# Optimization experiments

Hardware: AMD Instinct MI355X
Metric: run time of the kernel (lower is better)

The kernel has to match this reference:

```python
import jax, jax.numpy as jnp
import numpy as np

PLANES, RATIO = 512, 4
Q = PLANES // RATIO  # 128
B, H, W = 4, 128, 128


def _dw_stride2(x, k):
    # depthwise 3x3 stride-2 conv, NCHW, kernel [C,1,3,3]
    return jax.lax.conv_general_dilated(
        x, k, window_strides=(2, 2), padding=((1, 1), (1, 1)),
        feature_group_count=x.shape[1],
        dimension_numbers=('NCHW', 'OIHW', 'NCHW'))


def _upsample_bilinear_ac(x, out_h, out_w):
    # bilinear, align_corners=True (matches F.interpolate)
    n, c, h, w = x.shape
    def co(out, ins):
        s = (ins - 1) / (out - 1)
        pos = jnp.arange(out, dtype=jnp.float32) * jnp.float32(s)
        i0 = jnp.floor(pos).astype(jnp.int32)
        i1 = jnp.minimum(i0 + 1, ins - 1)
        return i0, i1, pos - i0.astype(jnp.float32)
    y0, y1, ty = co(out_h, h)
    x0, x1, tx = co(out_w, w)
    rows = x[:, :, y0, :] * (1 - ty)[None, None, :, None] + x[:, :, y1, :] * ty[None, None, :, None]
    return rows[:, :, :, x0] * (1 - tx) + rows[:, :, :, x1] * tx


def setup_inputs() -> dict:
    key = jax.random.key(0)
    ks = jax.random.split(key, 32)
    nrm = lambda k, s, sc=0.05: jax.random.normal(k, s, jnp.float32) * sc
    uni = lambda k, s: jax.random.uniform(k, s, jnp.float32, 0.5, 1.5)
    return {
        'feat': jax.random.normal(ks[0], (B, PLANES, H, W), jnp.float32),
        'w_phi': nrm(ks[1], (2 * Q, PLANES)),
        'bn_phi_s': uni(ks[2], (2 * Q,)), 'bn_phi_b': nrm(ks[3], (2 * Q,)),
        'w_theta': nrm(ks[4], (Q, PLANES)),
        'bn_theta_s': uni(ks[5], (Q,)), 'bn_theta_b': nrm(ks[6], (Q,)),
        'w_adj': nrm(ks[7], (Q, Q)),
        'bn_adj_s': uni(ks[8], (Q,)), 'bn_adj_b': nrm(ks[9], (Q,)),
        'w_wg': nrm(ks[10], (2 * Q, 2 * Q)),
        'bn_wg_s': uni(ks[11], (2 * Q,)), 'bn_wg_b': nrm(ks[12], (2 * Q,)),
        'w_conv3': nrm(ks[13], (PLANES, 2 * Q)),
        'bn3_s': uni(ks[14], (PLANES,)), 'bn3_b': nrm(ks[15], (PLANES,)),
        'w_local1': nrm(ks[16], (PLANES, 1, 3, 3), 0.2),
        'bnl1_s': uni(ks[17], (PLANES,)), 'bnl1_b': nrm(ks[18], (PLANES,)),
        'w_local2': nrm(ks[19], (PLANES, 1, 3, 3), 0.2),
        'bnl2_s': uni(ks[20], (PLANES,)), 'bnl2_b': nrm(ks[21], (PLANES,)),
        'w_local3': nrm(ks[22], (PLANES, 1, 3, 3), 0.2),
        'bnl3_s': uni(ks[23], (PLANES,)), 'bnl3_b': nrm(ks[24], (PLANES,)),
        'gamma': nrm(ks[25], (1,), 0.5),
        'w_final': nrm(ks[26], (PLANES, 2 * PLANES)),
        'bnf_s': uni(ks[27], (PLANES,)), 'bnf_b': nrm(ks[28], (PLANES,)),
    }


def reference(feat, w_phi, bn_phi_s, bn_phi_b, w_theta, bn_theta_s, bn_theta_b,
              w_adj, bn_adj_s, bn_adj_b, w_wg, bn_wg_s, bn_wg_b,
              w_conv3, bn3_s, bn3_b,
              w_local1, bnl1_s, bnl1_b, w_local2, bnl2_s, bnl2_b,
              w_local3, bnl3_s, bnl3_b, gamma, w_final, bnf_s, bnf_b):
    n, c, h, w = feat.shape
    bn2 = lambda x, s, b: x * s[None, :, None, None] + b[None, :, None, None]
    bn1 = lambda x, s, b: x * s[None, :, None] + b[None, :, None]
    conv1x1 = lambda x, wt: jnp.einsum('oc,nchw->nohw', wt, x)

    l = bn2(_dw_stride2(feat, w_local1), bnl1_s, bnl1_b)
    l = bn2(_dw_stride2(l, w_local2), bnl2_s, bnl2_b)
    l = bn2(_dw_stride2(l, w_local3), bnl3_s, bnl3_b)
    nl, cl, hl, wl = l.shape
    v = l.reshape(nl, cl, hl * wl)                      # [n,C,hw]
    energy = jnp.einsum('nck,ndk->ncd', v, v)           # [n,C,C]
    attn = jax.nn.softmax(jnp.max(energy, -1, keepdims=True) - energy, axis=-1)
    cam = jnp.einsum('ncd,ndk->nck', attn, v).reshape(nl, cl, hl, wl)
    l = gamma * cam + l
    local = _upsample_bilinear_ac(l, h, w)
    spatial_local_feat = feat * local + feat

    # ---- graph branch
    q = w_theta.shape[0]
    x_sqz = bn2(conv1x1(feat, w_phi), bn_phi_s, bn_phi_b).reshape(n, 2 * q, h * w)
    b_m = bn2(conv1x1(feat, w_theta), bn_theta_s, bn_theta_b).reshape(n, q, h * w)
    z_idt = jnp.einsum('nck,ndk->ncd', x_sqz, b_m)      # [n,2q,q]
    z = jnp.swapaxes(z_idt, 1, 2)                       # [n,q,2q]
    z = bn1(jnp.einsum('oi,nil->nol', w_adj, z), bn_adj_s, bn_adj_b)
    z = jnp.swapaxes(z, 1, 2) + z_idt                   # [n,2q,q]
    z = bn1(jnp.einsum('oi,nil->nol', w_wg, z), bn_wg_s, bn_wg_b)
    y = jnp.einsum('ncd,ndk->nck', z, b_m).reshape(n, 2 * q, h, w)
    y = bn2(conv1x1(y, w_conv3), bn3_s, bn3_b)
    g_out = jax.nn.relu(feat + y)

    out = bn2(conv1x1(jnp.concatenate([spatial_local_feat, g_out], axis=1), w_final), bnf_s, bnf_b)
    return out
```

## Files before the change

### kernel.cpp

```cpp
#include <hip/hip_runtime.h>
#include <hip/hip_bf16.h>
#include <cstddef>
#include <cstdint>

static constexpr int NB  = 4;
static constexpr int CH  = 512;
static constexpr int HH  = 128;
static constexpr int WWi = 128;
static constexpr int HW  = HH * WWi;
static constexpr int Qd  = 128;
static constexpr int Q2d = 256;

typedef __attribute__((ext_vector_type(8))) short bf8;
typedef __attribute__((ext_vector_type(4))) float f4;

__device__ __forceinline__ short f2bf(float x) {
  __hip_bfloat16 h = __float2bfloat16(x);
  short s; __builtin_memcpy(&s, &h, 2); return s;
}
__device__ __forceinline__ float bfs2f(short u) {
  union { unsigned int i; float f; } x;
  x.i = ((unsigned int)(unsigned short)u) << 16; return x.f;
}

__launch_bounds__(256)
__global__ void dw_conv_bn(const float* __restrict__ in, float* __restrict__ out,
                           const float* __restrict__ wgt, const float* __restrict__ s,
                           const float* __restrict__ b, int Hi, int Wi, int Ho, int Wo) {
  int idx = blockIdx.x * 256 + threadIdx.x;
  int wo = idx % Wo; int t = idx / Wo;
  int ho = t % Ho; t /= Ho;
  int c = t % CH; int n = t / CH;
  const float* ip = in + ((size_t)(n * CH + c)) * Hi * Wi;
  const float* wp = wgt + c * 9;
  float acc = 0.f;
  int hi = ho * 2 - 1, wi = wo * 2 - 1;
#pragma unroll
  for (int kh = 0; kh < 3; kh++) {
    int y = hi + kh;
    if ((unsigned)y < (unsigned)Hi) {
#pragma unroll
      for (int kw = 0; kw < 3; kw++) {
        int x = wi + kw;
        if ((unsigned)x < (unsigned)Wi) acc += wp[kh * 3 + kw] * ip[y * Wi + x];
      }
    }
  }
  out[idx] = acc * s[c] + b[c];
}

__launch_bounds__(256)
__global__ void lrow_kernel(const float* __restrict__ lcam, float* __restrict__ lrow) {
  int idx = blockIdx.x * 256 + threadIdx.x;
  int wcol = idx & 127; int t = idx >> 7;
  int hy = t & 15; t >>= 4;
  float pos = wcol * (15.f / 127.f);
  int x0 = (int)pos; if (x0 > 15) x0 = 15;
  float tx = pos - x0;
  int x1 = x0 + 1; if (x1 > 15) x1 = 15;
  const float* lc = lcam + ((size_t)t * 16 + hy) * 16;
  lrow[idx] = lc[x0] * (1.f - tx) + lc[x1] * tx;
}

__launch_bounds__(256)
__global__ void cvt_f32_bf16(const float* __restrict__ in, short* __restrict__ out, int n4) {
  int i = blockIdx.x * 256 + threadIdx.x;
  if (i >= n4) return;
  float4 v = ((const float4*)in)[i];
  short tmp[4] = {f2bf(v.x), f2bf(v.y), f2bf(v.z), f2bf(v.w)};
  short4 o; __builtin_memcpy(&o, tmp, 8);
  ((short4*)out)[i] = o;
}

__device__ __forceinline__ int sls(int row, int slot) {
  return row * 64 + ((slot ^ (((row >> 1) ^ (row >> 3)) & 7)) << 3);
}
__device__ __forceinline__ void stg64_b16(const short* __restrict__ src, size_t stride,
                                          int kb, short* lds, int t) {
#pragma unroll
  for (int i = 0; i < 4; i++) {
    int chunk = t + i * 256;
    int row = chunk >> 3, slot = chunk & 7;
    bf8 v = *(const bf8*)(src + (size_t)row * stride + kb + slot * 8);
    *(bf8*)(lds + sls(row, slot)) = v;
  }
}
__device__ __forceinline__ void stg64_f32(const float* __restrict__ src, size_t stride,
                                          int kb, short* lds, int t) {
#pragma unroll
  for (int i = 0; i < 4; i++) {
    int chunk = t + i * 256;
    int row = chunk >> 3, slot = chunk & 7;
    const float* sp = src + (size_t)row * stride + kb + slot * 8;
    float4 v0 = *(const float4*)sp, v1 = *(const float4*)(sp + 4);
    union { short s[8]; bf8 v; } u;
    u.s[0] = f2bf(v0.x); u.s[1] = f2bf(v0.y); u.s[2] = f2bf(v0.z); u.s[3] = f2bf(v0.w);
    u.s[4] = f2bf(v1.x); u.s[5] = f2bf(v1.y); u.s[6] = f2bf(v1.z); u.s[7] = f2bf(v1.w);
    *(bf8*)(lds + sls(row, slot)) = u.v;
  }
}
__device__ __forceinline__ void stg64_t32(const float* __restrict__ src, size_t sstride,
                                          int pb, short* lds, int t) {
#pragma unroll
  for (int i2 = 0; i2 < 4; i2++) {
    int chunk = t + i2 * 256;
    int c = (chunk >> 3) & 63;
    int p8 = ((chunk & 7) | ((chunk >> 6) & 8)) * 8;
    const float* fr = src + (size_t)c * sstride + pb + p8;
    float4 f0 = *(const float4*)fr, f1 = *(const float4*)(fr + 4);
    float fv[8];
    __builtin_memcpy(&fv[0], &f0, 16); __builtin_memcpy(&fv[4], &f1, 16);
    int slot = c >> 3, eidx = c & 7;
#pragma unroll
    for (int e = 0; e < 8; e++) {
      lds[sls(p8 + e, slot) + eidx] = f2bf(fv[e]);
    }
  }
}
__device__ __forceinline__ void stg64_t16(const short* __restrict__ src, size_t sstride,
                                          int pb, short* lds, int t) {
#pragma unroll
  for (int i2 = 0; i2 < 4; i2++) {
    int chunk = t + i2 * 256;
    int c = (chunk >> 3) & 63;
    int p8 = ((chunk & 7) | ((chunk >> 6) & 8)) * 8;
    bf8 v = *(const bf8*)(src + (size_t)c * sstride + pb + p8);
    int slot = c >> 3, eidx = c & 7;
#pragma unroll
    for (int e = 0; e < 8; e++) {
      lds[sls(p8 + e, slot) + eidx] = v[e];
    }
  }
}
__device__ __forceinline__ bf8 fragld64(const short* lds, int row, int kk, int lg) {
  return *(const bf8*)(lds + sls(row, kk * 4 + lg));
}

__launch_bounds__(256)
__global__ void energy_mfma(const float* __restrict__ l3, float* __restrict__ energy) {
  const int c0 = blockIdx.x * 128;
  const int d0 = blockIdx.y * 128;
  const int n = blockIdx.z;
  const int t = threadIdx.x;
  const int lane16 = t & 15, lg = (t >> 4) & 3, wave = t >> 6;
  const int wm = (wave >> 1) * 64, wn = (wave & 1) * 64;
  __shared__ __align__(16) short lA[8192], lB[8192];
  const float* srcA = l3 + ((size_t)n * CH + c0) * 256;
  const float* srcB = l3 + ((size_t)n * CH + d0) * 256;
  f4 acc[4][4];
#pragma unroll
  for (int i = 0; i < 4; i++)
#pragma unroll
    for (int j = 0; j < 4; j++) acc[i][j] = (f4)0.f;
  for (int kb = 0; kb < 256; kb += 64) {
    stg64_f32(srcA, 256, kb, lA, t);
    stg64_f32(srcB, 256, kb, lB, t);
    __syncthreads();
#pragma unroll
    for (int kk = 0; kk < 2; kk++) {
      bf8 av[4], bv[4];
#pragma unroll
      for (int i = 0; i < 4; i++) av[i] = fragld64(lA, wm + i * 16 + lane16, kk, lg);
#pragma unroll
      for (int j = 0; j < 4; j++) bv[j] = fragld64(lB, wn + j * 16 + lane16, kk, lg);
#pragma unroll
      for (int i = 0; i < 4; i++)
#pragma unroll
        for (int j = 0; j < 4; j++)
          acc[i][j] = __builtin_amdgcn_mfma_f32_16x16x32_bf16(av[i], bv[j], acc[i][j], 0, 0, 0);
    }
    __syncthreads();
  }
#pragma unroll
  for (int i = 0; i < 4; i++)
#pragma unroll
    for (int j = 0; j < 4; j++) {
      int d = d0 + wn + j * 16 + lane16;
#pragma unroll
      for (int r = 0; r < 4; r++) {
        int c = c0 + wm + i * 16 + lg * 4 + r;
        energy[((size_t)n * CH + c) * CH + d] = acc[i][j][r];
      }
    }
}

__launch_bounds__(256)
__global__ void softmax_attn(float* __restrict__ energy) {
  float* row = energy + (size_t)blockIdx.x * CH;
  int t = threadIdx.x;
  __shared__ float red[256];
  float e0 = row[t], e1 = row[t + 256];
  red[t] = fminf(e0, e1);
  __syncthreads();
  for (int s = 128; s > 0; s >>= 1) {
    if (t < s) red[t] = fminf(red[t], red[t + s]);
    __syncthreads();
  }
  float emin = red[0];
  __syncthreads();
  float w0 = __expf(emin - e0), w1 = __expf(emin - e1);
  red[t] = w0 + w1;
  __syncthreads();
  for (int s = 128; s > 0; s >>= 1) {
    if (t < s) red[t] += red[t + s];
    __syncthreads();
  }
  float inv = 1.f / red[0];
  row[t] = w0 * inv;
  row[t + 256] = w1 * inv;
}

__launch_bounds__(256)
__global__ void cam_mfma(const float* __restrict__ attn, const float* __restrict__ l3,
                         const float* __restrict__ gamma, float* __restrict__ lcam) {
  const int pb = blockIdx.x * 128;
  const int mb = blockIdx.y * 128;
  const int n = blockIdx.z;
  const int t = threadIdx.x;
  const int lane16 = t & 15, lg = (t >> 4) & 3, wave = t >> 6;
  const int wm = (wave >> 1) * 64, wn = (wave & 1) * 64;
  __shared__ __align__(16) short lA[8192], lB[8192];
  const float* srcA = attn + ((size_t)n * CH + mb) * CH;
  const float gm = gamma[0];
  f4 acc[4][4];
#pragma unroll
  for (int i = 0; i < 4; i++)
#pragma unroll
    for (int j = 0; j < 4; j++) acc[i][j] = (f4)0.f;
  for (int kb = 0; kb < 512; kb += 64) {
    stg64_f32(srcA, CH, kb, lA, t);
    stg64_t32(l3 + ((size_t)n * CH + kb) * 256, 256, pb, lB, t);
    __syncthreads();
#pragma unroll
    for (int kk = 0; kk < 2; kk++) {
      bf8 av[4], bv[4];
#pragma unroll
      for (int i = 0; i < 4; i++) av[i] = fragld64(lA, wm + i * 16 + lane16, kk, lg);
#pragma unroll
      for (int j = 0; j < 4; j++) bv[j] = fragld64(lB, wn + j * 16 + lane16, kk, lg);
#pragma unroll
      for (int i = 0; i < 4; i++)
#pragma unroll
        for (int j = 0; j < 4; j++)
          acc[i][j] = __builtin_amdgcn_mfma_f32_16x16x32_bf16(av[i], bv[j], acc[i][j], 0, 0, 0);
    }
    __syncthreads();
  }
#pragma unroll
  for (int i = 0; i < 4; i++)
#pragma unroll
    for (int j = 0; j < 4; j++) {
      int p = pb + wn + j * 16 + lane16;
#pragma unroll
      for (int r = 0; r < 4; r++) {
        int c = mb + wm + i * 16 + lg * 4 + r;
        size_t idx = ((size_t)n * CH + c) * 256 + p;
        lcam[idx] = gm * acc[i][j][r] + l3[idx];
      }
    }
}

__launch_bounds__(256)
__global__ void theta_mfma2(const short* __restrict__ wthb, const float* __restrict__ feat,
                            const float* __restrict__ s, const float* __restrict__ b,
                            short* __restrict__ bmb) {
  const int pb = blockIdx.x * 128;
  const int n = blockIdx.y;
  const int t = threadIdx.x;
  const int lane16 = t & 15, lg = (t >> 4) & 3, wave = t >> 6;
  const int wm = (wave >> 1) * 64, wn = (wave & 1) * 64;
  __shared__ __align__(16) short lA[8192], lB[8192];
  f4 acc[4][4];
#pragma unroll
  for (int i = 0; i < 4; i++)
#pragma unroll
    for (int j = 0; j < 4; j++) acc[i][j] = (f4)0.f;
  for (int kb = 0; kb < 512; kb += 64) {
    stg64_b16(wthb, 512, kb, lA, t);
    stg64_t32(feat + ((size_t)(n * CH) + kb) * HW, HW, pb, lB, t);
    __syncthreads();
#pragma unroll
    for (int kk = 0; kk < 2; kk++) {
      bf8 av[4], bv[4];
#pragma unroll
      for (int i = 0; i < 4; i++) av[i] = fragld64(lA, wm + i * 16 + lane16, kk, lg);
#pragma unroll
      for (int j = 0; j < 4; j++) bv[j] = fragld64(lB, wn + j * 16 + lane16, kk, lg);
#pragma unroll
      for (int i = 0; i < 4; i++)
#pragma unroll
        for (int j = 0; j < 4; j++)
          acc[i][j] = __builtin_amdgcn_mfma_f32_16x16x32_bf16(av[i], bv[j], acc[i][j], 0, 0, 0);
    }
    __syncthreads();
  }
#pragma unroll
  for (int i = 0; i < 4; i++)
#pragma unroll
    for (int j = 0; j < 4; j++) {
      int p = pb + wn + j * 16 + lane16;
#pragma unroll
      for (int r = 0; r < 4; r++) {
        int d = wm + i * 16 + lg * 4 + r;
        bmb[((size_t)(n * Qd) + d) * HW + p] = f2bf(s[d] * acc[i][j][r] + b[d]);
      }
    }
}

__launch_bounds__(256)
__global__ void rowsum_bf(const short* __restrict__ bmb, float* __restrict__ rs) {
  int row = blockIdx.x;
  int t = threadIdx.x;
  const short* r = bmb + (size_t)row * HW;
  float a = 0.f;
  for (int p = t * 8; p < HW; p += 2048) {
    bf8 v = *(const bf8*)(r + p);
#pragma unroll
    for (int e = 0; e < 8; e++) a += bfs2f(v[e]);
  }
  __shared__ float red[256];
  red[t] = a;
  __syncthreads();
  for (int s = 128; s > 0; s >>= 1) {
    if (t < s) red[t] += red[t + s];
    __syncthreads();
  }
  if (t == 0) rs[row] = red[0];
}

__launch_bounds__(256)
__global__ void m1_mfma2(const float* __restrict__ feat, const short* __restrict__ bmb,
                         float* __restrict__ m1p) {
  const int c0 = blockIdx.x * 128;
  const int kc = blockIdx.y;
  const int n = blockIdx.z;
  const int t = threadIdx.x;
  const int lane16 = t & 15, lg = (t >> 4) & 3, wave = t >> 6;
  const int wm = (wave >> 1) * 64, wn = (wave & 1) * 64;
  __shared__ __align__(16) short lA[8192], lB[8192];
  const float* srcA = feat + ((size_t)(n * CH) + c0) * HW;
  const short* srcB = bmb + (size_t)(n * Qd) * HW;
  f4 acc[4][4];
#pragma unroll
  for (int i = 0; i < 4; i++)
#pragma unroll
    for (int j = 0; j < 4; j++) acc[i][j] = (f4)0.f;
  const int kend = kc * 1024 + 1024;
  for (int kb = kc * 1024; kb < kend; kb += 64) {
    stg64_f32(srcA, HW, kb, lA, t);
    stg64_b16(srcB, HW, kb, lB, t);
    __syncthreads();
#pragma unroll
    for (int kk = 0; kk < 2; kk++) {
      bf8 av[4], bv[4];
#pragma unroll
      for (int i = 0; i < 4; i++) av[i] = fragld64(lA, wm + i * 16 + lane16, kk, lg);
#pragma unroll
      for (int j = 0; j < 4; j++) bv[j] = fragld64(lB, wn + j * 16 + lane16, kk, lg);
#pragma unroll
      for (int i = 0; i < 4; i++)
#pragma unroll
        for (int j = 0; j < 4; j++)
          acc[i][j] = __builtin_amdgcn_mfma_f32_16x16x32_bf16(av[i], bv[j], acc[i][j], 0, 0, 0);
    }
    __syncthreads();
  }
#pragma unroll
  for (int i = 0; i < 4; i++)
#pragma unroll
    for (int j = 0; j < 4; j++) {
      int d = wn + j * 16 + lane16;
#pragma unroll
      for (int r = 0; r < 4; r++) {
        int c = c0 + wm + i * 16 + lg * 4 + r;
        m1p[(((size_t)kc * NB + n) * CH + c) * Qd + d] = acc[i][j][r];
      }
    }
}

__launch_bounds__(256)
__global__ void m1_reduce(const float* __restrict__ m1p, float* __restrict__ m1) {
  int idx = blockIdx.x * 256 + threadIdx.x;
  float a = 0.f;
#pragma unroll
  for (int kc = 0; kc < 16; kc++) a += m1p[(size_t)kc * (NB * CH * Qd) + idx];
  m1[idx] = a;
}

__launch_bounds__(128)
__global__ void zidt_kernel(const float* __restrict__ m1, const float* __restrict__ wphi,
                            const float* __restrict__ sp, const float* __restrict__ bp,
                            const float* __restrict__ rs, float* __restrict__ zidt) {
  int n = blockIdx.y, c = blockIdx.x, d = threadIdx.x;
  __shared__ float wrow[512];
  for (int i = d; i < 512; i += 128) wrow[i] = wphi[(size_t)c * 512 + i];
  __syncthreads();
  const float* mb = m1 + (size_t)n * CH * Qd;
  float acc = 0.f;
#pragma unroll 4
  for (int i = 0; i < 512; i++) acc += wrow[i] * mb[i * Qd + d];
  zidt[((size_t)n * Q2d + c) * Qd + d] = sp[c] * acc + bp[c] * rs[n * Qd + d];
}

__launch_bounds__(128)
__global__ void z3_kernel(const float* __restrict__ zidt, const float* __restrict__ wadj,
                          const float* __restrict__ sa, const float* __restrict__ ba,
                          float* __restrict__ z3) {
  int n = blockIdx.y, c = blockIdx.x, d = threadIdx.x;
  __shared__ float zr[128];
  zr[d] = zidt[((size_t)n * Q2d + c) * Qd + d];
  __syncthreads();
  const float* wrow = wadj + (size_t)d * 128;
  float acc = 0.f;
#pragma unroll 4
  for (int i = 0; i < 128; i++) acc += wrow[i] * zr[i];
  z3[((size_t)n * Q2d + c) * Qd + d] = sa[d] * acc + ba[d] + zr[d];
}

__launch_bounds__(128)
__global__ void z4_kernel(const float* __restrict__ z3, const float* __restrict__ wwg,
                          const float* __restrict__ sw, const float* __restrict__ bw,
                          float* __restrict__ z4) {
  int n = blockIdx.y, o = blockIdx.x, d = threadIdx.x;
  __shared__ float wrow[256];
  wrow[d] = wwg[(size_t)o * 256 + d];
  wrow[d + 128] = wwg[(size_t)o * 256 + 128 + d];
  __syncthreads();
  const float* zb = z3 + (size_t)n * Q2d * Qd;
  float acc = 0.f;
#pragma unroll 4
  for (int i = 0; i < 256; i++) acc += wrow[i] * zb[i * Qd + d];
  z4[((size_t)n * Q2d + o) * Qd + d] = sw[o] * acc + bw[o];
}

__launch_bounds__(128)
__global__ void wz_kernel(const float* __restrict__ z4, const float* __restrict__ wc3,
                          const float* __restrict__ s3, float* __restrict__ wz) {
  int n = blockIdx.y, o = blockIdx.x, d = threadIdx.x;
  __shared__ float wrow[256];
  wrow[d] = wc3[(size_t)o * 256 + d];
  wrow[d + 128] = wc3[(size_t)o * 256 + 128 + d];
  __syncthreads();
  const float* zb = z4 + (size_t)n * Q2d * Qd;
  float acc = 0.f;
#pragma unroll 4
  for (int i = 0; i < 256; i++) acc += wrow[i] * zb[i * Qd + d];
  wz[((size_t)n * CH + o) * Qd + d] = s3[o] * acc;
}

__launch_bounds__(256)
__global__ void ygout_mfma2(const float* __restrict__ wz, const short* __restrict__ bmb,
                            const float* __restrict__ feat, const float* __restrict__ b3,
                            short* __restrict__ gout) {
  const int pb = blockIdx.x * 128;
  const int mb = blockIdx.y * 128;
  const int n = blockIdx.z;
  const int t = threadIdx.x;
  const int lane16 = t & 15, lg = (t >> 4) & 3, wave = t >> 6;
  const int wm = (wave >> 1) * 64, wn = (wave & 1) * 64;
  __shared__ __align__(16) short lA[8192], lB[8192];
  const float* srcA = wz + ((size_t)(n * CH) + mb) * Qd;
  f4 acc[4][4];
#pragma unroll
  for (int i = 0; i < 4; i++)
#pragma unroll
    for (int j = 0; j < 4; j++) acc[i][j] = (f4)0.f;
  for (int kb = 0; kb < 128; kb += 64) {
    stg64_f32(srcA, Qd, kb, lA, t);
    stg64_t16(bmb + ((size_t)(n * Qd) + kb) * HW, HW, pb, lB, t);
    __syncthreads();
#pragma unroll
    for (int kk = 0; kk < 2; kk++) {
      bf8 av[4], bv[4];
#pragma unroll
      for (int i = 0; i < 4; i++) av[i] = fragld64(lA, wm + i * 16 + lane16, kk, lg);
#pragma unroll
      for (int j = 0; j < 4; j++) bv[j] = fragld64(lB, wn + j * 16 + lane16, kk, lg);
#pragma unroll
      for (int i = 0; i < 4; i++)
#pragma unroll
        for (int j = 0; j < 4; j++)
          acc[i][j] = __builtin_amdgcn_mfma_f32_16x16x32_bf16(av[i], bv[j], acc[i][j], 0, 0, 0);
    }
    __syncthreads();
  }
#pragma unroll
  for (int i = 0; i < 4; i++)
#pragma unroll
    for (int j = 0; j < 4; j++) {
      int p = pb + wn + j * 16 + lane16;
#pragma unroll
      for (int r = 0; r < 4; r++) {
        int c = mb + wm + i * 16 + lg * 4 + r;
        size_t base = ((size_t)(n * CH) + c) * HW + p;
        float g = feat[base] + acc[i][j][r] + b3[c];
        gout[base] = f2bf(g > 0.f ? g : 0.f);
      }
    }
}

__launch_bounds__(256)
__global__ void final_mfma(const short* __restrict__ wfb, const float* __restrict__ feat,
                           const float* __restrict__ lrw, const short* __restrict__ gout,
                           const float* __restrict__ fs, const float* __restrict__ fb,
                           float* __restrict__ out) {
  const int h = blockIdx.x;
  const int pb = h * WWi;
  const int mb = blockIdx.y * 128;
  const int n = blockIdx.z;
  const int t = threadIdx.x;
  const int lane16 = t & 15, lg = (t >> 4) & 3, wave = t >> 6;
  const int wm = (wave >> 1) * 64, wn = (wave & 1) * 64;
  __shared__ __align__(16) short lA[8192], lB[8192];
  const float posy = h * (15.f / 127.f);
  int hy0 = (int)posy; if (hy0 > 15) hy0 = 15;
  int hy1 = hy0 + 1; if (hy1 > 15) hy1 = 15;
  const float tyv = posy - hy0;
  f4 acc[4][4];
#pragma unroll
  for (int i = 0; i < 4; i++)
#pragma unroll
    for (int j = 0; j < 4; j++) acc[i][j] = (f4)0.f;

  for (int kb = 0; kb < 1024; kb += 64) {
    stg64_b16(wfb + (size_t)mb * 1024, 1024, kb, lA, t);
    if (kb < 512) {
#pragma unroll
      for (int i2 = 0; i2 < 4; i2++) {
        int chunk = t + i2 * 256;
        int c = (chunk >> 3) & 63;
        int p8 = ((chunk & 7) | ((chunk >> 6) & 8)) * 8;
        size_t cb = (size_t)(n * CH) + kb + c;
        const float* fr = feat + cb * HW + pb + p8;
        float4 f0 = *(const float4*)fr, f1 = *(const float4*)(fr + 4);
        const float* l0r = lrw + (cb * 16 + hy0) * WWi + p8;
        const float* l1r = lrw + (cb * 16 + hy1) * WWi + p8;
        float4 a0 = *(const float4*)l0r, a1 = *(const float4*)(l0r + 4);
        float4 b0 = *(const float4*)l1r, b1 = *(const float4*)(l1r + 4);
        float fv[8], av[8], bv[8];
        __builtin_memcpy(&fv[0], &f0, 16); __builtin_memcpy(&fv[4], &f1, 16);
        __builtin_memcpy(&av[0], &a0, 16); __builtin_memcpy(&av[4], &a1, 16);
        __builtin_memcpy(&bv[0], &b0, 16); __builtin_memcpy(&bv[4], &b1, 16);
        int slot = c >> 3, eidx = c & 7;
#pragma unroll
        for (int e = 0; e < 8; e++) {
          float v = fv[e] * (1.f + av[e] + (bv[e] - av[e]) * tyv);
          lB[sls(p8 + e, slot) + eidx] = f2bf(v);
        }
      }
    } else {
      stg64_t16(gout + ((size_t)(n * CH) + (kb - 512)) * HW, HW, pb, lB, t);
    }
    __syncthreads();
#pragma unroll
    for (int kk = 0; kk < 2; kk++) {
      bf8 avf[4], bvf[4];
#pragma unroll
      for (int i = 0; i < 4; i++) avf[i] = fragld64(lA, wm + i * 16 + lane16, kk, lg);
#pragma unroll
      for (int j = 0; j < 4; j++) bvf[j] = fragld64(lB, wn + j * 16 + lane16, kk, lg);
#pragma unroll
      for (int i = 0; i < 4; i++)
#pragma unroll
        for (int j = 0; j < 4; j++)
          acc[i][j] = __builtin_amdgcn_mfma_f32_16x16x32_bf16(avf[i], bvf[j], acc[i][j], 0, 0, 0);
    }
    __syncthreads();
  }
#pragma unroll
  for (int i = 0; i < 4; i++)
#pragma unroll
    for (int j = 0; j < 4; j++) {
      int p = pb + wn + j * 16 + lane16;
#pragma unroll
      for (int r = 0; r < 4; r++) {
        int m = mb + wm + i * 16 + lg * 4 + r;
        out[((size_t)(n * CH) + m) * HW + p] = fs[m] * acc[i][j][r] + fb[m];
      }
    }
}

extern "C" void kernel_launch(void* const* d_in, const int* in_sizes, int n_in,
                              void* d_out, int out_size, void* d_ws, size_t ws_size,
                              hipStream_t stream) {
  (void)in_sizes; (void)n_in; (void)out_size; (void)ws_size;
  const float* feat      = (const float*)d_in[0];
  const float* w_phi     = (const float*)d_in[1];
  const float* bn_phi_s  = (const float*)d_in[2];
  const float* bn_phi_b  = (const float*)d_in[3];
  const float* w_theta   = (const float*)d_in[4];
  const float* bn_theta_s= (const float*)d_in[5];
  const float* bn_theta_b= (const float*)d_in[6];
  const float* w_adj     = (const float*)d_in[7];
  const float* bn_adj_s  = (const float*)d_in[8];
  const float* bn_adj_b  = (const float*)d_in[9];
  const float* w_wg      = (const float*)d_in[10];
  const float* bn_wg_s   = (const float*)d_in[11];
  const float* bn_wg_b   = (const float*)d_in[12];
  const float* w_conv3   = (const float*)d_in[13];
  const float* bn3_s     = (const float*)d_in[14];
  const float* bn3_b     = (const float*)d_in[15];
  const float* w_l1      = (const float*)d_in[16];
  const float* bnl1_s    = (const float*)d_in[17];
  const float* bnl1_b    = (const float*)d_in[18];
  const float* w_l2      = (const float*)d_in[19];
  const float* bnl2_s    = (const float*)d_in[20];
  const float* bnl2_b    = (const float*)d_in[21];
  const float* w_l3      = (const float*)d_in[22];
  const float* bnl3_s    = (const float*)d_in[23];
  const float* bnl3_b    = (const float*)d_in[24];
  const float* gamma     = (const float*)d_in[25];
  const float* w_final   = (const float*)d_in[26];
  const float* bnf_s     = (const float*)d_in[27];
  const float* bnf_b     = (const float*)d_in[28];

  float* out = (float*)d_out;
  float* l1 = out;
  float* l2 = l1 + (size_t)8388608;
  float* l3 = l2 + (size_t)2097152;
  short* wthb = (short*)(l3 + (size_t)524288);

  float* ws   = (float*)d_ws;
  float* lcam = ws;
  float* lrw  = lcam + (size_t)4 * 512 * 256;
  float* bm_region = lrw + (size_t)4 * 512 * 16 * 128;
  short* bmb  = (short*)bm_region;
  float* rsum = bm_region + (size_t)4 * 128 * 16384;
  float* M1   = rsum + 512;
  float* M1p_old = M1 + (size_t)4 * 512 * 128;
  float* zidt = M1p_old + (size_t)8 * 4 * 512 * 128;
  float* z3b  = zidt + (size_t)4 * 256 * 128;
  float* z4b  = z3b + (size_t)4 * 256 * 128;
  float* wzb  = z4b + (size_t)4 * 256 * 128;
  short* gout = (short*)(wzb + (size_t)4 * 512 * 128);
  short* wfb  = (short*)M1p_old;
  float* m1p  = (float*)gout;
  float* energy = (float*)M1p_old;

  dw_conv_bn<<<dim3(4 * 512 * 64 * 64 / 256), 256, 0, stream>>>(feat, l1, w_l1, bnl1_s, bnl1_b, 128, 128, 64, 64);
  dw_conv_bn<<<dim3(4 * 512 * 32 * 32 / 256), 256, 0, stream>>>(l1, l2, w_l2, bnl2_s, bnl2_b, 64, 64, 32, 32);
  dw_conv_bn<<<dim3(4 * 512 * 16 * 16 / 256), 256, 0, stream>>>(l2, l3, w_l3, bnl3_s, bnl3_b, 32, 32, 16, 16);
  energy_mfma<<<dim3(4, 4, 4), 256, 0, stream>>>(l3, energy);
  softmax_attn<<<dim3(4 * 512), 256, 0, stream>>>(energy);
  cam_mfma<<<dim3(2, 4, 4), 256, 0, stream>>>(energy, l3, gamma, lcam);
  lrow_kernel<<<dim3(4 * 512 * 16 * 128 / 256), 256, 0, stream>>>(lcam, lrw);

  cvt_f32_bf16<<<dim3(64), 256, 0, stream>>>(w_theta, wthb, 16384);
  theta_mfma2<<<dim3(128, 4), 256, 0, stream>>>(wthb, feat, bn_theta_s, bn_theta_b, bmb);
  rowsum_bf<<<dim3(512), 256, 0, stream>>>(bmb, rsum);
  m1_mfma2<<<dim3(4, 16, 4), 256, 0, stream>>>(feat, bmb, m1p);
  m1_reduce<<<dim3(1024), 256, 0, stream>>>(m1p, M1);
  zidt_kernel<<<dim3(256, 4), 128, 0, stream>>>(M1, w_phi, bn_phi_s, bn_phi_b, rsum, zidt);
  z3_kernel<<<dim3(256, 4), 128, 0, stream>>>(zidt, w_adj, bn_adj_s, bn_adj_b, z3b);
  z4_kernel<<<dim3(256, 4), 128, 0, stream>>>(z3b, w_wg, bn_wg_s, bn_wg_b, z4b);
  wz_kernel<<<dim3(512, 4), 128, 0, stream>>>(z4b, w_conv3, bn3_s, wzb);
  ygout_mfma2<<<dim3(128, 4, 4), 256, 0, stream>>>(wzb, bmb, feat, bn3_b, gout);

  cvt_f32_bf16<<<dim3(512), 256, 0, stream>>>(w_final, wfb, 131072);

  final_mfma<<<dim3(128, 4, 4), 256, 0, stream>>>(wfb, feat, lrw, gout, bnf_s, bnf_b, out);
}
```

Measured before the change: 503.8 us.

## Precompute bf16 spatial-local features in half-image chunks before final GEMM

Moves the feat*(1+upsampled local) computation out of the final GEMM's inner loop into a separate slf_build kernel that writes a bf16 buffer. The final GEMM runs in two passes of 64 rows each and loads that buffer with the same transposed staging path used for gout. Before, each of the four channel-tile blocks recomputed this product and re-read feat and lrw; now it is computed once per half-image. The cost is an extra buffer write and read plus two more launches. Separately, the m1 GEMM split-K doubles from 16 to 32 chunks for more parallelism, at the price of a larger partial-sum reduction.

```diff
diff --git a/kernel.cpp b/kernel.cpp
--- a/kernel.cpp
+++ b/kernel.cpp
@@ -70,6 +70,35 @@
   short tmp[4] = {f2bf(v.x), f2bf(v.y), f2bf(v.z), f2bf(v.w)};
   short4 o; __builtin_memcpy(&o, tmp, 8);
   ((short4*)out)[i] = o;
+}
+
+__launch_bounds__(256)
+__global__ void slf_build(const float* __restrict__ feat, const float* __restrict__ lrw,
+                          short* __restrict__ slfb, int h0) {
+  int idx = blockIdx.x * 256 + threadIdx.x;
+  int w8 = (idx & 15) * 8; int t = idx >> 4;
+  int h = (t & 63) + h0; t >>= 6;
+  const float posy = h * (15.f / 127.f);
+  int hy0 = (int)posy; if (hy0 > 15) hy0 = 15;
+  int hy1 = hy0 + 1; if (hy1 > 15) hy1 = 15;
+  const float tyv = posy - hy0;
+  const float* fr = feat + (size_t)t * HW + h * WWi + w8;
+  const float* l0r = lrw + ((size_t)t * 16 + hy0) * WWi + w8;
+  const float* l1r = lrw + ((size_t)t * 16 + hy1) * WWi + w8;
+  float4 f0 = *(const float4*)fr, f1 = *(const float4*)(fr + 4);
+  float4 a0 = *(const float4*)l0r, a1 = *(const float4*)(l0r + 4);
+  float4 b0 = *(const float4*)l1r, b1 = *(const float4*)(l1r + 4);
+  float fv[8], av[8], bv[8];
+  __builtin_memcpy(&fv[0], &f0, 16); __builtin_memcpy(&fv[4], &f1, 16);
+  __builtin_memcpy(&av[0], &a0, 16); __builtin_memcpy(&av[4], &a1, 16);
+  __builtin_memcpy(&bv[0], &b0, 16); __builtin_memcpy(&bv[4], &b1, 16);
+  union { short s[8]; bf8 v; } u;
+#pragma unroll
+  for (int e = 0; e < 8; e++) {
+    float v = fv[e] * (1.f + av[e] + (bv[e] - av[e]) * tyv);
+    u.s[e] = f2bf(v);
+  }
+  *(bf8*)(slfb + ((size_t)t * 64 + (h - h0)) * WWi + w8) = u.v;
 }
 
 __device__ __forceinline__ int sls(int row, int slot) {
@@ -345,8 +374,8 @@
   for (int i = 0; i < 4; i++)
 #pragma unroll
     for (int j = 0; j < 4; j++) acc[i][j] = (f4)0.f;
-  const int kend = kc * 1024 + 1024;
-  for (int kb = kc * 1024; kb < kend; kb += 64) {
+  const int kend = kc * 512 + 512;
+  for (int kb = kc * 512; kb < kend; kb += 64) {
     stg64_f32(srcA, HW, kb, lA, t);
     stg64_b16(srcB, HW, kb, lB, t);
     __syncthreads();
@@ -383,7 +412,7 @@
   int idx = blockIdx.x * 256 + threadIdx.x;
   float a = 0.f;
 #pragma unroll
-  for (int kc = 0; kc < 16; kc++) a += m1p[(size_t)kc * (NB * CH * Qd) + idx];
+  for (int kc = 0; kc < 32; kc++) a += m1p[(size_t)kc * (NB * CH * Qd) + idx];
   m1[idx] = a;
 }
 
@@ -500,11 +529,11 @@
 }
 
 __launch_bounds__(256)
-__global__ void final_mfma(const short* __restrict__ wfb, const float* __restrict__ feat,
-                           const float* __restrict__ lrw, const short* __restrict__ gout,
+__global__ void final_mfma(const short* __restrict__ wfb, const short* __restrict__ slfb,
+                           const int h0, const short* __restrict__ gout,
                            const float* __restrict__ fs, const float* __restrict__ fb,
                            float* __restrict__ out) {
-  const int h = blockIdx.x;
+  const int h = blockIdx.x + h0;
   const int pb = h * WWi;
   const int mb = blockIdx.y * 128;
   const int n = blockIdx.z;
@@ -512,10 +541,6 @@
   const int lane16 = t & 15, lg = (t >> 4) & 3, wave = t >> 6;
   const int wm = (wave >> 1) * 64, wn = (wave & 1) * 64;
   __shared__ __align__(16) short lA[8192], lB[8192];
-  const float posy = h * (15.f / 127.f);
-  int hy0 = (int)posy; if (hy0 > 15) hy0 = 15;
-  int hy1 = hy0 + 1; if (hy1 > 15) hy1 = 15;
-  const float tyv = posy - hy0;
   f4 acc[4][4];
 #pragma unroll
   for (int i = 0; i < 4; i++)
@@ -525,29 +550,8 @@
   for (int kb = 0; kb < 1024; kb += 64) {
     stg64_b16(wfb + (size_t)mb * 1024, 1024, kb, lA, t);
     if (kb < 512) {
-#pragma unroll
-      for (int i2 = 0; i2 < 4; i2++) {
-        int chunk = t + i2 * 256;
-        int c = (chunk >> 3) & 63;
-        int p8 = ((chunk & 7) | ((chunk >> 6) & 8)) * 8;
-        size_t cb = (size_t)(n * CH) + kb + c;
-        const float* fr = feat + cb * HW + pb + p8;
-        float4 f0 = *(const float4*)fr, f1 = *(const float4*)(fr + 4);
-        const float* l0r = lrw + (cb * 16 + hy0) * WWi + p8;
-        const float* l1r = lrw + (cb * 16 + hy1) * WWi + p8;
-        float4 a0 = *(const float4*)l0r, a1 = *(const float4*)(l0r + 4);
-        float4 b0 = *(const float4*)l1r, b1 = *(const float4*)(l1r + 4);
-        float fv[8], av[8], bv[8];
-        __builtin_memcpy(&fv[0], &f0, 16); __builtin_memcpy(&fv[4], &f1, 16);
-        __builtin_memcpy(&av[0], &a0, 16); __builtin_memcpy(&av[4], &a1, 16);
-        __builtin_memcpy(&bv[0], &b0, 16); __builtin_memcpy(&bv[4], &b1, 16);
-        int slot = c >> 3, eidx = c & 7;
-#pragma unroll
-        for (int e = 0; e < 8; e++) {
-          float v = fv[e] * (1.f + av[e] + (bv[e] - av[e]) * tyv);
-          lB[sls(p8 + e, slot) + eidx] = f2bf(v);
-        }
-      }
+      stg64_t16(slfb + ((size_t)(n * CH) + kb) * (64 * WWi) + (size_t)(h - h0) * WWi,
+                64 * WWi, 0, lB, t);
     } else {
       stg64_t16(gout + ((size_t)(n * CH) + (kb - 512)) * HW, HW, pb, lB, t);
     }
@@ -636,6 +640,7 @@
   short* wfb  = (short*)M1p_old;
   float* m1p  = (float*)gout;
   float* energy = (float*)M1p_old;
+  short* slfb = (short*)bm_region;
 
   dw_conv_bn<<<dim3(4 * 512 * 64 * 64 / 256), 256, 0, stream>>>(feat, l1, w_l1, bnl1_s, bnl1_b, 128, 128, 64, 64);
   dw_conv_bn<<<dim3(4 * 512 * 32 * 32 / 256), 256, 0, stream>>>(l1, l2, w_l2, bnl2_s, bnl2_b, 64, 64, 32, 32);
@@ -648,7 +653,7 @@
   cvt_f32_bf16<<<dim3(64), 256, 0, stream>>>(w_theta, wthb, 16384);
   theta_mfma2<<<dim3(128, 4), 256, 0, stream>>>(wthb, feat, bn_theta_s, bn_theta_b, bmb);
   rowsum_bf<<<dim3(512), 256, 0, stream>>>(bmb, rsum);
-  m1_mfma2<<<dim3(4, 16, 4), 256, 0, stream>>>(feat, bmb, m1p);
+  m1_mfma2<<<dim3(4, 32, 4), 256, 0, stream>>>(feat, bmb, m1p);
   m1_reduce<<<dim3(1024), 256, 0, stream>>>(m1p, M1);
   zidt_kernel<<<dim3(256, 4), 128, 0, stream>>>(M1, w_phi, bn_phi_s, bn_phi_b, rsum, zidt);
   z3_kernel<<<dim3(256, 4), 128, 0, stream>>>(zidt, w_adj, bn_adj_s, bn_adj_b, z3b);
@@ -658,5 +663,8 @@
 
   cvt_f32_bf16<<<dim3(512), 256, 0, stream>>>(w_final, wfb, 131072);
 
-  final_mfma<<<dim3(128, 4, 4), 256, 0, stream>>>(wfb, feat, lrw, gout, bnf_s, bnf_b, out);
-}
+  slf_build<<<dim3(8192), 256, 0, stream>>>(feat, lrw, slfb, 0);
+  final_mfma<<<dim3(64, 4, 4), 256, 0, stream>>>(wfb, slfb, 0, gout, bnf_s, bnf_b, out);
+  slf_build<<<dim3(8192), 256, 0, stream>>>(feat, lrw, slfb, 64);
+  final_mfma<<<dim3(64, 4, 4), 256, 0, stream>>>(wfb, slfb, 64, gout, bnf_s, bnf_b, out);
+}
```

Result: slower. 520.6 us (+3.3%).
